# Optimization experiments

Measured on AMD Instinct MI355X. Metric: run time of the kernel, lower is better.

Reference implementation:

```python
import jax, jax.numpy as jnp
import numpy as np

NUM_HEADS = 8
LN_EPS = 1e-6


def _layer_norm(x, gamma, beta):
    mu = jnp.mean(x, axis=-1, keepdims=True)
    var = jnp.mean(jnp.square(x - mu), axis=-1, keepdims=True)
    return (x - mu) / jnp.sqrt(var + LN_EPS) * gamma + beta


def setup_inputs() -> dict:
    key = jax.random.key(0)
    B, S, H, F = 4, 2048, 1024, 4096
    ks = jax.random.split(key, 12)
    scale = 1.0 / np.sqrt(H)
    x = jax.random.normal(ks[0], (B, S, H), dtype=jnp.float32)
    # additive padding mask: 1 where masked, 0 where attended
    mask = jax.random.randint(ks[1], (B, 1, 1, S), 0, 2).astype(jnp.float32)
    Wq = jax.random.normal(ks[2], (H, H), dtype=jnp.float32) * scale
    Wk = jax.random.normal(ks[3], (H, H), dtype=jnp.float32) * scale
    Wv = jax.random.normal(ks[4], (H, H), dtype=jnp.float32) * scale
    Wo = jax.random.normal(ks[5], (H, H), dtype=jnp.float32) * scale
    W1 = jax.random.normal(ks[6], (H, F), dtype=jnp.float32) * scale
    b1 = jnp.zeros((F,), dtype=jnp.float32)
    W2 = jax.random.normal(ks[7], (F, H), dtype=jnp.float32) * (1.0 / np.sqrt(F))
    b2 = jnp.zeros((H,), dtype=jnp.float32)
    gamma = jnp.ones((H,), dtype=jnp.float32)
    beta = jnp.zeros((H,), dtype=jnp.float32)
    return {"x": x, "mask": mask, "Wq": Wq, "Wk": Wk, "Wv": Wv, "Wo": Wo,
            "W1": W1, "b1": b1, "W2": W2, "b2": b2, "gamma": gamma, "beta": beta}


def reference(x, mask, Wq, Wk, Wv, Wo, W1, b1, W2, b2, gamma, beta):
    B, S, H = x.shape
    nh = NUM_HEADS
    d = H // nh

    def split_heads(t):
        return t.reshape(B, S, nh, d).transpose(0, 2, 1, 3)  # [B,nh,S,d]

    q = split_heads(x @ Wq)
    k = split_heads(x @ Wk)
    v = split_heads(x @ Wv)

    # FAITHFUL to source bug: score /= d**(-0.5)  ==  score * sqrt(d)
    scores = jnp.einsum('bhqd,bhkd->bhqk', q, k) * jnp.sqrt(jnp.float32(d))
    scores = scores + mask * (-1e9)
    attn = jax.nn.softmax(scores, axis=-1)
    ctx = jnp.einsum('bhqk,bhkd->bhqd', attn, v)
    ctx = ctx.transpose(0, 2, 1, 3).reshape(B, S, H)
    attn_out = ctx @ Wo

    # dropout = identity (eval mode)
    x = _layer_norm(x + attn_out, gamma, beta)
    ffn = jnp.maximum(x @ W1 + b1, 0.0) @ W2 + b2
    x = _layer_norm(x + ffn, gamma, beta)
    return x
```

## Files before the change

kernel.cpp:

```cpp
#include <hip/hip_runtime.h>


typedef __bf16 bf16;
typedef __bf16 bf16x4 __attribute__((ext_vector_type(4)));
typedef __bf16 bf16x8 __attribute__((ext_vector_type(8)));
typedef float  f32x4  __attribute__((ext_vector_type(4)));

#define MFMA16(a, b, c) __builtin_amdgcn_mfma_f32_16x16x32_bf16(a, b, c, 0, 0, 0)

typedef const __attribute__((address_space(1))) void* gas_cptr;
typedef __attribute__((address_space(3))) void* las_ptr;

__device__ __forceinline__ void g2l16(const void* g, void* l) {
    __builtin_amdgcn_global_load_lds((gas_cptr)g, (las_ptr)l, 16, 0, 0);
}

__device__ __forceinline__ uint b16bits(bf16 v) {
    union { bf16 h; unsigned short u; } cv; cv.h = v; return (uint)cv.u;
}

__global__ __launch_bounds__(256) void split_f32_k(
    const float* __restrict__ in, bf16* __restrict__ hi, bf16* __restrict__ lo)
{
    const long i = (long)blockIdx.x * 256 + threadIdx.x;
    const float4 v = *(const float4*)(in + i * 4);
    const float a[4] = {v.x, v.y, v.z, v.w};
    bf16x4 h, l;
#pragma unroll
    for (int j = 0; j < 4; j++) {
        h[j] = (bf16)a[j];
        l[j] = (bf16)(a[j] - (float)h[j]);
    }
    *(bf16x4*)(hi + i * 4) = h;
    *(bf16x4*)(lo + i * 4) = l;
}

__global__ __launch_bounds__(256) void transpose_f32_k(
    const float* __restrict__ in, bf16* __restrict__ out_hi, bf16* __restrict__ out_lo,
    int in_rs, int out_rs)
{
    __shared__ uint Th[64][33];
    __shared__ uint Tl[64][33];
    const long c0 = (long)blockIdx.x * 64;
    const long r0 = (long)blockIdx.y * 64;
    const int t = threadIdx.x, rp = t >> 3, cc = t & 7;
    const float* pa = in + (r0 + 2 * rp) * (long)in_rs + c0 + cc * 8;
    const float* pb = pa + in_rs;
    float a[8], b[8];
    *(float4*)&a[0] = *(const float4*)pa;
    *(float4*)&a[4] = *(const float4*)(pa + 4);
    *(float4*)&b[0] = *(const float4*)pb;
    *(float4*)&b[4] = *(const float4*)(pb + 4);
#pragma unroll
    for (int j = 0; j < 8; j++) {
        const bf16 ah = (bf16)a[j], bh = (bf16)b[j];
        Th[cc * 8 + j][rp] = b16bits(ah) | (b16bits(bh) << 16);
        const bf16 al = (bf16)(a[j] - (float)ah), bl = (bf16)(b[j] - (float)bh);
        Tl[cc * 8 + j][rp] = b16bits(al) | (b16bits(bl) << 16);
    }
    __syncthreads();
#pragma unroll
    for (int i = 0; i < 2; i++) {
        const int task = i * 256 + t;
        const int c = task >> 3, ch = task & 7;
        uint4 wv;
        wv.x = Th[c][ch * 4 + 0]; wv.y = Th[c][ch * 4 + 1];
        wv.z = Th[c][ch * 4 + 2]; wv.w = Th[c][ch * 4 + 3];
        *(uint4*)(out_hi + (c0 + c) * (long)out_rs + r0 + ch * 8) = wv;
        if (out_lo) {
            uint4 wl;
            wl.x = Tl[c][ch * 4 + 0]; wl.y = Tl[c][ch * 4 + 1];
            wl.z = Tl[c][ch * 4 + 2]; wl.w = Tl[c][ch * 4 + 3];
            *(uint4*)(out_lo + (c0 + c) * (long)out_rs + r0 + ch * 8) = wl;
        }
    }
}

__global__ __launch_bounds__(256) void transpose_bf16_k(
    const bf16* __restrict__ in, bf16* __restrict__ out,
    int in_rs, int out_rs, int nh, long bo_in, long bi_in, long bo_out)
{
    __shared__ uint T[64][33];
    const int z = blockIdx.z;
    const bf16* inp = in + (long)(z / nh) * bo_in + (long)(z % nh) * bi_in;
    bf16* outp = out + (long)z * bo_out;
    const long c0 = (long)blockIdx.x * 64;
    const long r0 = (long)blockIdx.y * 64;
    const int t = threadIdx.x, rp = t >> 3, cc = t & 7;

    const uint4 ra = *(const uint4*)(inp + (r0 + 2 * rp) * (long)in_rs + c0 + cc * 8);
    const uint4 rb = *(const uint4*)(inp + (r0 + 2 * rp + 1) * (long)in_rs + c0 + cc * 8);
    const uint a32[4] = {ra.x, ra.y, ra.z, ra.w};
    const uint b32[4] = {rb.x, rb.y, rb.z, rb.w};
#pragma unroll
    for (int j = 0; j < 8; j++) {
        const uint av = (j & 1) ? (a32[j >> 1] >> 16) : (a32[j >> 1] & 0xffffu);
        const uint bv = (j & 1) ? (b32[j >> 1] >> 16) : (b32[j >> 1] & 0xffffu);
        T[cc * 8 + j][rp] = av | (bv << 16);
    }
    __syncthreads();
#pragma unroll
    for (int i = 0; i < 2; i++) {
        const int task = i * 256 + t;
        const int c = task >> 3, ch = task & 7;
        uint4 wv;
        wv.x = T[c][ch * 4 + 0]; wv.y = T[c][ch * 4 + 1];
        wv.z = T[c][ch * 4 + 2]; wv.w = T[c][ch * 4 + 3];
        *(uint4*)(outp + (c0 + c) * (long)out_rs + r0 + ch * 8) = wv;
    }
}

__global__ __launch_bounds__(256) void gemm_bf16_k(
    const bf16* __restrict__ A, const bf16* __restrict__ Bt,
    bf16* __restrict__ out,
    const float* __restrict__ bias, int relu, int M, int N, int K)
{
    __shared__ __align__(16) bf16 As[128 * 32];
    __shared__ __align__(16) bf16 Bs[128 * 32];
    const int t = threadIdx.x;
    const int fr = t & 15, fq = (t >> 4) & 3;
    const int w = t >> 6, wm = w & 1, wn = w >> 1;
    const long mBase = (long)blockIdx.y * 128;
    const long nBase = (long)blockIdx.x * 128;

    f32x4 acc[4][4];
#pragma unroll
    for (int i = 0; i < 4; i++)
#pragma unroll
        for (int j = 0; j < 4; j++) acc[i][j] = (f32x4){0.f, 0.f, 0.f, 0.f};

    const int arow = t >> 2;
    const int akc  = (t & 3) * 8;
    const bf16* ga0 = A + (mBase + arow) * (long)K + akc;
    const bf16* ga1 = A + (mBase + arow + 64) * (long)K + akc;
    const bf16* gb0 = Bt + (nBase + arow) * (long)K + akc;
    const bf16* gb1 = Bt + (nBase + arow + 64) * (long)K + akc;
    bf16* la0 = &As[t * 8];
    bf16* la1 = &As[(256 + t) * 8];
    bf16* lb0 = &Bs[t * 8];
    bf16* lb1 = &Bs[(256 + t) * 8];

    const int aoff = (wm * 64 + fr) * 32 + fq * 8;
    const int boff = (wn * 64 + fr) * 32 + fq * 8;

    for (int kt = 0; kt < K; kt += 32) {
        g2l16(ga0 + kt, la0);
        g2l16(ga1 + kt, la1);
        g2l16(gb0 + kt, lb0);
        g2l16(gb1 + kt, lb1);
        __syncthreads();
        bf16x8 af[4], bfv[4];
#pragma unroll
        for (int mt = 0; mt < 4; mt++) af[mt] = *(const bf16x8*)&As[aoff + mt * 512];
#pragma unroll
        for (int nt = 0; nt < 4; nt++) bfv[nt] = *(const bf16x8*)&Bs[boff + nt * 512];
#pragma unroll
        for (int mt = 0; mt < 4; mt++)
#pragma unroll
            for (int nt = 0; nt < 4; nt++)
                acc[mt][nt] = MFMA16(af[mt], bfv[nt], acc[mt][nt]);
        __syncthreads();
    }

    const long crow0 = mBase + wm * 64;
    const long ccol0 = nBase + wn * 64;
#pragma unroll
    for (int nt = 0; nt < 4; nt++) {
        const long col = ccol0 + nt * 16 + fr;
        const float bv = bias ? bias[col] : 0.0f;
#pragma unroll
        for (int mt = 0; mt < 4; mt++)
#pragma unroll
            for (int r = 0; r < 4; r++) {
                const long rowg = crow0 + mt * 16 + fq * 4 + r;
                float v = acc[mt][nt][r] + bv;
                if (relu) v = fmaxf(v, 0.0f);
                out[rowg * (long)N + col] = (bf16)v;
            }
    }
}

__global__ __launch_bounds__(256) void gemm_split_k(
    const bf16* __restrict__ Ah, const bf16* __restrict__ Al,
    const bf16* __restrict__ Bh, const bf16* __restrict__ Bl,
    bf16* __restrict__ out_hi, bf16* __restrict__ out_lo, int M, int N, int K)
{
    __shared__ __align__(16) bf16 Ahs[128 * 32];
    __shared__ __align__(16) bf16 Als[128 * 32];
    __shared__ __align__(16) bf16 Bhs[128 * 32];
    __shared__ __align__(16) bf16 Bls[128 * 32];
    const int t = threadIdx.x;
    const int fr = t & 15, fq = (t >> 4) & 3;
    const int w = t >> 6, wm = w & 1, wn = w >> 1;
    const long mBase = (long)blockIdx.y * 128;
    const long nBase = (long)blockIdx.x * 128;

    f32x4 acc[4][4];
#pragma unroll
    for (int i = 0; i < 4; i++)
#pragma unroll
        for (int j = 0; j < 4; j++) acc[i][j] = (f32x4){0.f, 0.f, 0.f, 0.f};

    const int arow = t >> 2;
    const int akc  = (t & 3) * 8;
    const long ga0 = (mBase + arow) * (long)K + akc;
    const long ga1 = (mBase + arow + 64) * (long)K + akc;
    const long gb0 = (nBase + arow) * (long)K + akc;
    const long gb1 = (nBase + arow + 64) * (long)K + akc;

    const int aoff = (wm * 64 + fr) * 32 + fq * 8;
    const int boff = (wn * 64 + fr) * 32 + fq * 8;

    for (int kt = 0; kt < K; kt += 32) {
        g2l16(Ah + ga0 + kt, &Ahs[t * 8]);
        g2l16(Ah + ga1 + kt, &Ahs[(256 + t) * 8]);
        g2l16(Al + ga0 + kt, &Als[t * 8]);
        g2l16(Al + ga1 + kt, &Als[(256 + t) * 8]);
        g2l16(Bh + gb0 + kt, &Bhs[t * 8]);
        g2l16(Bh + gb1 + kt, &Bhs[(256 + t) * 8]);
        g2l16(Bl + gb0 + kt, &Bls[t * 8]);
        g2l16(Bl + gb1 + kt, &Bls[(256 + t) * 8]);
        __syncthreads();
        bf16x8 ah[4], al[4], bh[4], bl[4];
#pragma unroll
        for (int mt = 0; mt < 4; mt++) {
            ah[mt] = *(const bf16x8*)&Ahs[aoff + mt * 512];
            al[mt] = *(const bf16x8*)&Als[aoff + mt * 512];
        }
#pragma unroll
        for (int nt = 0; nt < 4; nt++) {
            bh[nt] = *(const bf16x8*)&Bhs[boff + nt * 512];
            bl[nt] = *(const bf16x8*)&Bls[boff + nt * 512];
        }
#pragma unroll
        for (int mt = 0; mt < 4; mt++)
#pragma unroll
            for (int nt = 0; nt < 4; nt++) {
                acc[mt][nt] = MFMA16(ah[mt], bh[nt], acc[mt][nt]);
                acc[mt][nt] = MFMA16(ah[mt], bl[nt], acc[mt][nt]);
                acc[mt][nt] = MFMA16(al[mt], bh[nt], acc[mt][nt]);
            }
        __syncthreads();
    }

    const long crow0 = mBase + wm * 64;
    const long ccol0 = nBase + wn * 64;
#pragma unroll
    for (int nt = 0; nt < 4; nt++) {
        const long col = ccol0 + nt * 16 + fr;
#pragma unroll
        for (int mt = 0; mt < 4; mt++)
#pragma unroll
            for (int r = 0; r < 4; r++) {
                const long rowg = crow0 + mt * 16 + fq * 4 + r;
                const float v = acc[mt][nt][r];
                const long idx = rowg * (long)N + col;
                const bf16 h = (bf16)v;
                out_hi[idx] = h;
                out_lo[idx] = (bf16)(v - (float)h);
            }
    }
}

#define KROW 132
#define VROW 68
#define PROW 68
__global__ __launch_bounds__(256, 2) void flash_attn_k(
    const bf16* __restrict__ qhi, const bf16* __restrict__ qlo,
    const bf16* __restrict__ khi, const bf16* __restrict__ klo,
    const bf16* __restrict__ vt, const float* __restrict__ mask,
    bf16* __restrict__ ctx)
{
    __shared__ __align__(16) bf16 Kh[64 * KROW];
    __shared__ __align__(16) bf16 Kl[64 * KROW];
    __shared__ __align__(16) bf16 Vs[128 * VROW];
    __shared__ __align__(16) bf16 Ps[4][16 * PROW];
    const float scale = 11.3137085f;
    const int t = threadIdx.x, w = t >> 6;
    const int fr = t & 15, fq = (t >> 4) & 3;
    const int blk = blockIdx.x;
    const int qt = blk & 15, bh_ = blk >> 4, b = bh_ >> 3, h = bh_ & 7;
    const int qrow0 = qt * 128 + w * 16;

    bf16x8 qh[2][4], ql[2][4];
#pragma unroll
    for (int mt = 0; mt < 2; mt++) {
        const long qoff = ((long)(b * 2048 + qrow0 + mt * 64 + fr)) * 1024 + h * 128 + fq * 8;
#pragma unroll
        for (int s = 0; s < 4; s++) {
            qh[mt][s] = *(const bf16x8*)(qhi + qoff + s * 32);
            ql[mt][s] = *(const bf16x8*)(qlo + qoff + s * 32);
        }
    }
    f32x4 o[2][8];
#pragma unroll
    for (int mt = 0; mt < 2; mt++)
#pragma unroll
        for (int nt = 0; nt < 8; nt++) o[mt][nt] = (f32x4){0.f, 0.f, 0.f, 0.f};
    float m_run[2][4], l_run[2][4];
#pragma unroll
    for (int mt = 0; mt < 2; mt++)
#pragma unroll
        for (int r = 0; r < 4; r++) { m_run[mt][r] = -1e30f; l_run[mt][r] = 0.f; }

    const long kbase = (long)(b * 2048) * 1024 + h * 128 + (long)(t & 15) * 8;
    const long vbase = ((long)bh_ * 128) * 2048 + (long)(t & 7) * 8;
    const float* maskb = mask + b * 2048;

    for (int kt = 0; kt < 32; kt++) {
        __syncthreads();
#pragma unroll
        for (int i = 0; i < 4; i++) {
            const int key = i * 16 + (t >> 4);
            const long g = kbase + (long)(kt * 64 + key) * 1024;
            const bf16x8 vk_h = *(const bf16x8*)(khi + g);
            const bf16x8 vk_l = *(const bf16x8*)(klo + g);
            const int d = i * 32 + (t >> 3);
            const bf16x8 vv = *(const bf16x8*)(vt + vbase + (long)d * 2048 + kt * 64);
            *(bf16x8*)&Kh[key * KROW + (t & 15) * 8] = vk_h;
            *(bf16x8*)&Kl[key * KROW + (t & 15) * 8] = vk_l;
            *(bf16x8*)&Vs[d * VROW + (t & 7) * 8] = vv;
        }
        float madd[4];
#pragma unroll
        for (int ct = 0; ct < 4; ct++)
            madd[ct] = maskb[kt * 64 + ct * 16 + fr] * (-1e9f);
        __syncthreads();

        f32x4 sc[2][4];
#pragma unroll
        for (int mt = 0; mt < 2; mt++)
#pragma unroll
            for (int ct = 0; ct < 4; ct++) sc[mt][ct] = (f32x4){0.f, 0.f, 0.f, 0.f};
        __builtin_amdgcn_s_setprio(1);
#pragma unroll
        for (int s = 0; s < 4; s++)
#pragma unroll
            for (int ct = 0; ct < 4; ct++) {
                const int off = (ct * 16 + fr) * KROW + s * 32 + fq * 8;
                const bf16x8 kh8 = *(const bf16x8*)&Kh[off];
                const bf16x8 kl8 = *(const bf16x8*)&Kl[off];
#pragma unroll
                for (int mt = 0; mt < 2; mt++) {
                    sc[mt][ct] = MFMA16(qh[mt][s], kh8, sc[mt][ct]);
                    sc[mt][ct] = MFMA16(qh[mt][s], kl8, sc[mt][ct]);
                    sc[mt][ct] = MFMA16(ql[mt][s], kh8, sc[mt][ct]);
                }
            }
        __builtin_amdgcn_s_setprio(0);

#pragma unroll
        for (int mt = 0; mt < 2; mt++) {
            float alpha[4];
#pragma unroll
            for (int r = 0; r < 4; r++) {
                float mx = sc[mt][0][r] * scale + madd[0];
                mx = fmaxf(mx, sc[mt][1][r] * scale + madd[1]);
                mx = fmaxf(mx, sc[mt][2][r] * scale + madd[2]);
                mx = fmaxf(mx, sc[mt][3][r] * scale + madd[3]);
                mx = fmaxf(mx, __shfl_xor(mx, 1));
                mx = fmaxf(mx, __shfl_xor(mx, 2));
                mx = fmaxf(mx, __shfl_xor(mx, 4));
                mx = fmaxf(mx, __shfl_xor(mx, 8));
                const float mn = fmaxf(m_run[mt][r], mx);
                alpha[r] = __expf(m_run[mt][r] - mn);
                m_run[mt][r] = mn;
            }
            float lt[4] = {0.f, 0.f, 0.f, 0.f};
#pragma unroll
            for (int ct = 0; ct < 4; ct++)
#pragma unroll
                for (int r = 0; r < 4; r++) {
                    const float p = __expf(sc[mt][ct][r] * scale + madd[ct] - m_run[mt][r]);
                    lt[r] += p;
                    Ps[w][(fq * 4 + r) * PROW + ct * 16 + fr] = (bf16)p;
                }
#pragma unroll
            for (int r = 0; r < 4; r++) {
                float s_ = lt[r];
                s_ += __shfl_xor(s_, 1); s_ += __shfl_xor(s_, 2);
                s_ += __shfl_xor(s_, 4); s_ += __shfl_xor(s_, 8);
                l_run[mt][r] = l_run[mt][r] * alpha[r] + s_;
            }
            const int need = (alpha[0] < 1.f) | (alpha[1] < 1.f) |
                             (alpha[2] < 1.f) | (alpha[3] < 1.f);
            if (__any(need)) {
#pragma unroll
                for (int nt = 0; nt < 8; nt++)
#pragma unroll
                    for (int r = 0; r < 4; r++) o[mt][nt][r] *= alpha[r];
            }

            __builtin_amdgcn_s_setprio(1);
#pragma unroll
            for (int sp = 0; sp < 2; sp++) {
                const bf16x8 pf = *(const bf16x8*)&Ps[w][fr * PROW + sp * 32 + fq * 8];
#pragma unroll
                for (int nt = 0; nt < 8; nt++) {
                    const bf16x8 vf = *(const bf16x8*)&Vs[(nt * 16 + fr) * VROW + sp * 32 + fq * 8];
                    o[mt][nt] = MFMA16(pf, vf, o[mt][nt]);
                }
            }
            __builtin_amdgcn_s_setprio(0);
        }
    }
#pragma unroll
    for (int mt = 0; mt < 2; mt++)
#pragma unroll
        for (int r = 0; r < 4; r++) {
            const float inv = l_run[mt][r] > 0.f ? 1.0f / l_run[mt][r] : 0.f;
#pragma unroll
            for (int nt = 0; nt < 8; nt++) {
                const long idx = ((long)(b * 2048 + qrow0 + mt * 64 + fq * 4 + r)) * 1024
                               + h * 128 + nt * 16 + fr;
                ctx[idx] = (bf16)(o[mt][nt][r] * inv);
            }
        }
}

__global__ __launch_bounds__(256) void add_ln_k(
    const float* __restrict__ xf, const bf16* __restrict__ y,
    const float* __restrict__ gamma, const float* __restrict__ beta,
    float* __restrict__ out, bf16* __restrict__ out_b)
{
    __shared__ float red[8];
    const long row = blockIdx.x;
    const int t = threadIdx.x, lane = t & 63, w = t >> 6;
    float v[4];
    const float4 xv = *(const float4*)(xf + row * 1024 + t * 4);
    v[0] = xv.x; v[1] = xv.y; v[2] = xv.z; v[3] = xv.w;
    const bf16x4 yv = *(const bf16x4*)(y + row * 1024 + t * 4);
    float s = 0.f, s2 = 0.f;
#pragma unroll
    for (int i = 0; i < 4; i++) {
        v[i] += (float)yv[i];
        s += v[i]; s2 += v[i] * v[i];
    }
#pragma unroll
    for (int off = 1; off < 64; off <<= 1) {
        s += __shfl_xor(s, off);
        s2 += __shfl_xor(s2, off);
    }
    if (lane == 0) { red[w] = s; red[4 + w] = s2; }
    __syncthreads();
    s = red[0] + red[1] + red[2] + red[3];
    s2 = red[4] + red[5] + red[6] + red[7];
    const float mean = s * (1.0f / 1024.0f);
    const float var = s2 * (1.0f / 1024.0f) - mean * mean;
    const float rstd = rsqrtf(var + 1e-6f);
    float4 ov;
    ov.x = (v[0] - mean) * rstd * gamma[t * 4 + 0] + beta[t * 4 + 0];
    ov.y = (v[1] - mean) * rstd * gamma[t * 4 + 1] + beta[t * 4 + 1];
    ov.z = (v[2] - mean) * rstd * gamma[t * 4 + 2] + beta[t * 4 + 2];
    ov.w = (v[3] - mean) * rstd * gamma[t * 4 + 3] + beta[t * 4 + 3];
    *(float4*)(out + row * 1024 + t * 4) = ov;
    if (out_b) {
        bf16x4 hb;
        hb[0] = (bf16)ov.x; hb[1] = (bf16)ov.y; hb[2] = (bf16)ov.z; hb[3] = (bf16)ov.w;
        *(bf16x4*)(out_b + row * 1024 + t * 4) = hb;
    }
}

extern "C" void kernel_launch(void* const* d_in, const int* in_sizes, int n_in,
                              void* d_out, int out_size, void* d_ws, size_t ws_size,
                              hipStream_t stream)
{
    (void)in_sizes; (void)n_in; (void)out_size; (void)ws_size;
    const float* x     = (const float*)d_in[0];
    const float* mask  = (const float*)d_in[1];
    const float* Wq    = (const float*)d_in[2];
    const float* Wk    = (const float*)d_in[3];
    const float* Wv    = (const float*)d_in[4];
    const float* Wo    = (const float*)d_in[5];
    const float* W1    = (const float*)d_in[6];
    const float* b1    = (const float*)d_in[7];
    const float* W2    = (const float*)d_in[8];
    const float* b2    = (const float*)d_in[9];
    const float* gamma = (const float*)d_in[10];
    const float* beta  = (const float*)d_in[11];
    float* out = (float*)d_out;

    char* ws = (char*)d_ws;
    const size_t SZ = 8192ul * 1024 * 2;
    bf16* qhi  = (bf16*)(ws + 0 * SZ);
    bf16* qlo  = (bf16*)(ws + 1 * SZ);
    bf16* khi  = (bf16*)(ws + 2 * SZ);
    bf16* klo  = (bf16*)(ws + 3 * SZ);
    bf16* hbuf = (bf16*)(ws + 0 * SZ);
    bf16* vbuf = (bf16*)(ws + 4 * SZ);
    bf16* ctxb = vbuf;
    bf16* vtb  = (bf16*)(ws + 5 * SZ);
    bf16* fbuf = vtb;
    bf16* xh   = (bf16*)(ws + 6 * SZ);
    bf16* xl   = (bf16*)(ws + 7 * SZ);
    bf16* aob  = xl;
    float* x1f = (float*)(ws + 8 * SZ);
    bf16* x1b  = (bf16*)(ws + 10 * SZ);
    char* wts  = ws + 11 * SZ;
    bf16* Wqth = (bf16*)(wts);
    bf16* Wqtl = (bf16*)(wts + 1 * 2097152);
    bf16* Wkth = (bf16*)(wts + 2 * 2097152);
    bf16* Wktl = (bf16*)(wts + 3 * 2097152);
    bf16* Wvt  = (bf16*)(wts + 4 * 2097152);
    bf16* Wot  = (bf16*)(wts + 5 * 2097152);
    bf16* W1t  = (bf16*)(wts + 6 * 2097152);
    bf16* W2t  = (bf16*)(wts + 6 * 2097152 + 8388608);

    const dim3 blk(256);
    split_f32_k<<<dim3(8192), blk, 0, stream>>>(x, xh, xl);
    transpose_f32_k<<<dim3(16, 16), blk, 0, stream>>>(Wq, Wqth, Wqtl, 1024, 1024);
    transpose_f32_k<<<dim3(16, 16), blk, 0, stream>>>(Wk, Wkth, Wktl, 1024, 1024);
    transpose_f32_k<<<dim3(16, 16), blk, 0, stream>>>(Wv, Wvt, nullptr, 1024, 1024);
    transpose_f32_k<<<dim3(16, 16), blk, 0, stream>>>(Wo, Wot, nullptr, 1024, 1024);
    transpose_f32_k<<<dim3(64, 16), blk, 0, stream>>>(W1, W1t, nullptr, 4096, 1024);
    transpose_f32_k<<<dim3(16, 64), blk, 0, stream>>>(W2, W2t, nullptr, 1024, 4096);
    gemm_split_k<<<dim3(8, 64), blk, 0, stream>>>(xh, xl, Wqth, Wqtl, qhi, qlo, 8192, 1024, 1024);
    gemm_split_k<<<dim3(8, 64), blk, 0, stream>>>(xh, xl, Wkth, Wktl, khi, klo, 8192, 1024, 1024);
    gemm_bf16_k<<<dim3(8, 64), blk, 0, stream>>>(xh, Wvt, vbuf, nullptr, 0, 8192, 1024, 1024);
    transpose_bf16_k<<<dim3(2, 32, 32), blk, 0, stream>>>(vbuf, vtb, 1024, 2048, 8,
                                                          (long)2048 * 1024, 128L, (long)128 * 2048);
    flash_attn_k<<<dim3(512), blk, 0, stream>>>(qhi, qlo, khi, klo, vtb, mask, ctxb);
    gemm_bf16_k<<<dim3(8, 64), blk, 0, stream>>>(ctxb, Wot, aob, nullptr, 0, 8192, 1024, 1024);
    add_ln_k<<<dim3(8192), blk, 0, stream>>>(x, aob, gamma, beta, x1f, x1b);
    gemm_bf16_k<<<dim3(32, 64), blk, 0, stream>>>(x1b, W1t, hbuf, b1, 1, 8192, 4096, 1024);
    gemm_bf16_k<<<dim3(8, 64), blk, 0, stream>>>(hbuf, W2t, fbuf, b2, 0, 8192, 1024, 4096);
    add_ln_k<<<dim3(8192), blk, 0, stream>>>(x1f, fbuf, gamma, beta, out, nullptr);
}
```

Measured before the change: 764.6 us.

## Compact unmasked keys per batch and skip masked key tiles in attention

Adds a mask scan kernel that builds, for each batch, a compacted list of unmasked key indices and their count. The V transpose gathers rows through this list, and flash attention iterates only over tiles of kept keys, gathering K rows by index and masking only the padded tail. Masked keys get exp(-1e9) and contribute nothing, so skipping them preserves the result except when a row is fully masked. It saves about half the attention work on random masks, at the cost of indirect gathers and an extra small kernel.

```diff
diff --git a/kernel.cpp b/kernel.cpp
--- a/kernel.cpp
+++ b/kernel.cpp
@@ -33,6 +33,42 @@
     }
     *(bf16x4*)(hi + i * 4) = h;
     *(bf16x4*)(lo + i * 4) = l;
+}
+
+__global__ __launch_bounds__(256) void mask_scan_k(
+    const float* __restrict__ mask, unsigned short* __restrict__ cidx,
+    int* __restrict__ nbuf)
+{
+    __shared__ int wsum[4];
+    const int b = blockIdx.x, t = threadIdx.x;
+    const int lane = t & 63, w = t >> 6;
+    float m[8];
+    *(float4*)&m[0] = *(const float4*)(mask + b * 2048 + t * 8);
+    *(float4*)&m[4] = *(const float4*)(mask + b * 2048 + t * 8 + 4);
+    int keep[8], cnt = 0;
+#pragma unroll
+    for (int j = 0; j < 8; j++) {
+        keep[j] = (m[j] < 0.5f) ? 1 : 0;
+        cnt += keep[j];
+    }
+    int pre = cnt;
+#pragma unroll
+    for (int off = 1; off < 64; off <<= 1) {
+        const int nv = __shfl_up(pre, off);
+        if (lane >= off) pre += nv;
+    }
+    if (lane == 63) wsum[w] = pre;
+    __syncthreads();
+    int base = 0;
+    for (int i = 0; i < w; i++) base += wsum[i];
+    const int total = wsum[0] + wsum[1] + wsum[2] + wsum[3];
+    int p = base + pre - cnt;
+#pragma unroll
+    for (int j = 0; j < 8; j++)
+        if (keep[j]) cidx[b * 2048 + (p++)] = (unsigned short)(t * 8 + j);
+    for (int j = t; j < 2048; j += 256)
+        if (j >= total) cidx[b * 2048 + j] = 0;
+    if (t == 0) nbuf[b] = total;
 }
 
 __global__ __launch_bounds__(256) void transpose_f32_k(
@@ -78,18 +114,29 @@
 
 __global__ __launch_bounds__(256) void transpose_bf16_k(
     const bf16* __restrict__ in, bf16* __restrict__ out,
-    int in_rs, int out_rs, int nh, long bo_in, long bi_in, long bo_out)
+    int in_rs, int out_rs, int nh, long bo_in, long bi_in, long bo_out,
+    const unsigned short* __restrict__ cidx, const int* __restrict__ nbuf)
 {
     __shared__ uint T[64][33];
     const int z = blockIdx.z;
-    const bf16* inp = in + (long)(z / nh) * bo_in + (long)(z % nh) * bi_in;
+    const int bb = z / nh;
+    const long r0 = (long)blockIdx.y * 64;
+    if (nbuf) {
+        const int npad = (nbuf[bb] + 63) & ~63;
+        if (r0 >= npad) return;
+    }
+    const bf16* inp = in + (long)bb * bo_in + (long)(z % nh) * bi_in;
     bf16* outp = out + (long)z * bo_out;
     const long c0 = (long)blockIdx.x * 64;
-    const long r0 = (long)blockIdx.y * 64;
     const int t = threadIdx.x, rp = t >> 3, cc = t & 7;
 
-    const uint4 ra = *(const uint4*)(inp + (r0 + 2 * rp) * (long)in_rs + c0 + cc * 8);
-    const uint4 rb = *(const uint4*)(inp + (r0 + 2 * rp + 1) * (long)in_rs + c0 + cc * 8);
+    long ra_i = r0 + 2 * rp, rb_i = ra_i + 1;
+    if (cidx) {
+        ra_i = cidx[bb * 2048 + ra_i];
+        rb_i = cidx[bb * 2048 + rb_i];
+    }
+    const uint4 ra = *(const uint4*)(inp + ra_i * (long)in_rs + c0 + cc * 8);
+    const uint4 rb = *(const uint4*)(inp + rb_i * (long)in_rs + c0 + cc * 8);
     const uint a32[4] = {ra.x, ra.y, ra.z, ra.w};
     const uint b32[4] = {rb.x, rb.y, rb.z, rb.w};
 #pragma unroll
@@ -268,13 +315,15 @@
 __global__ __launch_bounds__(256, 2) void flash_attn_k(
     const bf16* __restrict__ qhi, const bf16* __restrict__ qlo,
     const bf16* __restrict__ khi, const bf16* __restrict__ klo,
-    const bf16* __restrict__ vt, const float* __restrict__ mask,
+    const bf16* __restrict__ vt,
+    const unsigned short* __restrict__ cidx, const int* __restrict__ nbuf,
     bf16* __restrict__ ctx)
 {
     __shared__ __align__(16) bf16 Kh[64 * KROW];
     __shared__ __align__(16) bf16 Kl[64 * KROW];
     __shared__ __align__(16) bf16 Vs[128 * VROW];
     __shared__ __align__(16) bf16 Ps[4][16 * PROW];
+    __shared__ __align__(16) unsigned short CI[2048];
     const float scale = 11.3137085f;
     const int t = threadIdx.x, w = t >> 6;
     const int fr = t & 15, fq = (t >> 4) & 3;
@@ -282,6 +331,10 @@
     const int qt = blk & 15, bh_ = blk >> 4, b = bh_ >> 3, h = bh_ & 7;
     const int qrow0 = qt * 128 + w * 16;
 
+    const int nB = nbuf[b];
+    const int ntiles = (nB + 63) >> 6;
+    *(uint4*)&CI[t * 8] = *(const uint4*)(cidx + (long)b * 2048 + t * 8);
+
     bf16x8 qh[2][4], ql[2][4];
 #pragma unroll
     for (int mt = 0; mt < 2; mt++) {
@@ -305,14 +358,14 @@
 
     const long kbase = (long)(b * 2048) * 1024 + h * 128 + (long)(t & 15) * 8;
     const long vbase = ((long)bh_ * 128) * 2048 + (long)(t & 7) * 8;
-    const float* maskb = mask + b * 2048;
-
-    for (int kt = 0; kt < 32; kt++) {
+
+    for (int kt = 0; kt < ntiles; kt++) {
         __syncthreads();
 #pragma unroll
         for (int i = 0; i < 4; i++) {
             const int key = i * 16 + (t >> 4);
-            const long g = kbase + (long)(kt * 64 + key) * 1024;
+            const int srow = CI[kt * 64 + key];
+            const long g = kbase + (long)srow * 1024;
             const bf16x8 vk_h = *(const bf16x8*)(khi + g);
             const bf16x8 vk_l = *(const bf16x8*)(klo + g);
             const int d = i * 32 + (t >> 3);
@@ -324,7 +377,7 @@
         float madd[4];
 #pragma unroll
         for (int ct = 0; ct < 4; ct++)
-            madd[ct] = maskb[kt * 64 + ct * 16 + fr] * (-1e9f);
+            madd[ct] = (kt * 64 + ct * 16 + fr < nB) ? 0.0f : -1e9f;
         __syncthreads();
 
         f32x4 sc[2][4];
@@ -505,9 +558,12 @@
     bf16* Wot  = (bf16*)(wts + 5 * 2097152);
     bf16* W1t  = (bf16*)(wts + 6 * 2097152);
     bf16* W2t  = (bf16*)(wts + 6 * 2097152 + 8388608);
+    unsigned short* cidxb = (unsigned short*)(wts + 6 * 2097152 + 2 * 8388608);
+    int* nbuf = (int*)((char*)cidxb + 4 * 2048 * sizeof(unsigned short));
 
     const dim3 blk(256);
     split_f32_k<<<dim3(8192), blk, 0, stream>>>(x, xh, xl);
+    mask_scan_k<<<dim3(4), blk, 0, stream>>>(mask, cidxb, nbuf);
     transpose_f32_k<<<dim3(16, 16), blk, 0, stream>>>(Wq, Wqth, Wqtl, 1024, 1024);
     transpose_f32_k<<<dim3(16, 16), blk, 0, stream>>>(Wk, Wkth, Wktl, 1024, 1024);
     transpose_f32_k<<<dim3(16, 16), blk, 0, stream>>>(Wv, Wvt, nullptr, 1024, 1024);
@@ -518,8 +574,9 @@
     gemm_split_k<<<dim3(8, 64), blk, 0, stream>>>(xh, xl, Wkth, Wktl, khi, klo, 8192, 1024, 1024);
     gemm_bf16_k<<<dim3(8, 64), blk, 0, stream>>>(xh, Wvt, vbuf, nullptr, 0, 8192, 1024, 1024);
     transpose_bf16_k<<<dim3(2, 32, 32), blk, 0, stream>>>(vbuf, vtb, 1024, 2048, 8,
-                                                          (long)2048 * 1024, 128L, (long)128 * 2048);
-    flash_attn_k<<<dim3(512), blk, 0, stream>>>(qhi, qlo, khi, klo, vtb, mask, ctxb);
+                                                          (long)2048 * 1024, 128L, (long)128 * 2048,
+                                                          cidxb, nbuf);
+    flash_attn_k<<<dim3(512), blk, 0, stream>>>(qhi, qlo, khi, klo, vtb, cidxb, nbuf, ctxb);
     gemm_bf16_k<<<dim3(8, 64), blk, 0, stream>>>(ctxb, Wot, aob, nullptr, 0, 8192, 1024, 1024);
     add_ln_k<<<dim3(8192), blk, 0, stream>>>(x, aob, gamma, beta, x1f, x1b);
     gemm_bf16_k<<<dim3(32, 64), blk, 0, stream>>>(x1b, W1t, hbuf, b1, 1, 8192, 4096, 1024);
```

Measured after the change: 672.7 us. -12.0%, faster.
